# Performance work log

Measured on AMD Instinct MI355X. Metric: run time of the kernel, lower is better.

The kernel has to match this reference:

```python
import jax, jax.numpy as jnp
import numpy as np

T, B, H, W = 4, 8, 480, 640
N = 4_000_000


def setup_inputs() -> dict:
    key = jax.random.key(0)
    k1, k2, k3, k4 = jax.random.split(key, 4)
    # sorted batch ids (events grouped per sample)
    batch = jnp.sort(jax.random.randint(k1, (N,), 0, B)).astype(jnp.int32)
    # x,y normalized to [0,1]; t sorted globally => sorted within each batch
    xy = jax.random.uniform(k2, (N, 2), dtype=jnp.float32)
    t = jnp.sort(jax.random.uniform(k3, (N,), dtype=jnp.float32))
    pos = jnp.concatenate([xy, t[:, None]], axis=1)  # [N,3]
    feat = jax.random.normal(k4, (N, 1), dtype=jnp.float32)  # polarity = feat[:,0] > 0
    return {"pos": pos, "feat": feat, "batch": batch}


def _voxelize(pos, feat, batch):
    n = pos.shape[0]
    bids = jnp.arange(B, dtype=batch.dtype)
    left = jnp.searchsorted(batch, bids, side="left")
    right = jnporig = jnp.searchsorted(batch, bids, side="right")
    first = jnp.clip(left, 0, n - 1)
    last = jnp.clip(right - 1, 0, n - 1)

    t = pos[:, 2]
    cnt = right - left
    # torch: if t[-1] == t[0] (and >=2 events), bump last event's t by 1
    bump = ((cnt >= 2) & (t[last] == t[first])).astype(t.dtype)
    t = t.at[last].add(bump)

    t0b = t[first]                       # per-batch t[0]
    denom = t[last] - t0b                # per-batch t[-1]-t[0]
    denom = jnp.where(denom == 0, 1.0, denom)  # guard degenerate segments
    tn = (T - 1) * (t - t0b[batch]) / denom[batch]  # [N]

    xf = pos[:, 0] * (W - 1)
    yf = pos[:, 1] * (H - 1)
    x0 = xf.astype(jnp.int32)
    y0 = yf.astype(jnp.int32)
    t0 = tn.astype(jnp.int32)
    ch = jnp.where(feat[:, 0] > 0, 0, 1).astype(jnp.int32)  # pos->chan0, neg->chan1

    # 8 trilinear corners: offsets in {0,1}^3, shape [8,1] broadcast vs [N]
    offs = jnp.array([[dx, dy, dt] for dx in (0, 1) for dy in (0, 1) for dt in (0, 1)], dtype=jnp.int32)
    xl = x0[None, :] + offs[:, 0:1]  # [8,N]
    yl = y0[None, :] + offs[:, 1:2]
    tl = t0[None, :] + offs[:, 2:3]

    m = (xl >= 0) & (xl < W) & (yl >= 0) & (yl < H) & (tl >= 0) & (tl < T)
    w = (1 - jnp.abs(xl - xf[None, :])) * (1 - jnp.abs(yl - yf[None, :])) * (1 - jnp.abs(tl - tn[None, :]))

    bb = batch[None, :].astype(jnp.int32)
    idx = (((tl * B + bb) * 2 + ch[None, :]) * H + yl) * W + xl  # flat into [T,B,2,H,W]
    idx = jnp.where(m, idx, 0)
    w = jnp.where(m, w, 0.0)

    out = jnp.zeros(T * B * 2 * H * W, dtype=jnp.float32).at[idx.ravel()].add(w.ravel())
    return out.reshape(T, B, 2, H, W)


def reference(pos, feat, batch) -> jnp.ndarray:
    return _voxelize(pos, feat, batch)
```

## Files before the change

kernel.cpp:

```cpp
#include <hip/hip_runtime.h>

#define TT 4
#define BB 8
#define HH 480
#define WW 640
#define YSTR 4
#define NYB (HH/YSTR)
#define NBINS2 (BB*TT*NYB)
#define CAP2 1792
#define PPB2 2048
#define FTH 512
#define ITER (PPB2/FTH)
#define SBINS 1024
#define RROWS 4
#define NSTRIPE (HH/RROWS)
#define GTH 512
#define FXSCALE 524288.0f
#define FXINV (1.0f/524288.0f)

struct BatchParams { float t0b; float denom; int last; int bump; };

__global__ void setup_kernel(const float* __restrict__ pos, const int* __restrict__ batch,
                             int n, BatchParams* __restrict__ bp) {
    int b = threadIdx.x;
    if (b >= BB) return;
    int lo = 0, hi = n;
    while (lo < hi) { int mid = (lo + hi) >> 1; if (batch[mid] < b) lo = mid + 1; else hi = mid; }
    int left = lo;
    lo = left; hi = n;
    while (lo < hi) { int mid = (lo + hi) >> 1; if (batch[mid] <= b) lo = mid + 1; else hi = mid; }
    int right = lo;
    int first = min(max(left, 0), n - 1);
    int last  = min(max(right - 1, 0), n - 1);
    int cnt   = right - left;
    float tf = pos[(size_t)first * 3 + 2];
    float tl = pos[(size_t)last  * 3 + 2];
    int bump = (cnt >= 2 && tl == tf) ? 1 : 0;
    float d = (tl + (float)bump) - tf;
    if (d == 0.0f) d = 1.0f;
    bp[b].t0b = tf; bp[b].denom = d; bp[b].last = last; bp[b].bump = bump;
}

__device__ __forceinline__ int point_g(const BatchParams* sbp, const float* pos,
                                       const int* batch, int i, float* tn_out) {
    int b = batch[i];
    float t = pos[(size_t)i * 3 + 2];
    BatchParams p = sbp[b];
    if (p.bump && i == p.last) t += 1.0f;
    float tn = (float)(TT - 1) * (t - p.t0b) / p.denom;
    *tn_out = tn;
    return b * TT + (int)tn;
}

__global__ __launch_bounds__(FTH) void fill4_kernel(
        const float* __restrict__ pos, const float* __restrict__ feat,
        const int* __restrict__ batch, const BatchParams* __restrict__ bp,
        unsigned int* __restrict__ cursor, uint2* __restrict__ binidx, int n) {
    __shared__ uint2 stage[PPB2];
    __shared__ unsigned int addrbuf[PPB2];
    __shared__ unsigned int hist[SBINS];
    __shared__ int          dlt[SBINS];
    __shared__ unsigned int ps[FTH];
    __shared__ unsigned int totloc;
    __shared__ BatchParams sbp[BB];
    int tid = threadIdx.x;
    if (tid < BB) sbp[tid] = bp[tid];
    hist[tid] = 0; hist[tid + FTH] = 0;
    __syncthreads();

    int lo = blockIdx.x * PPB2;
    float tnd;
    int g_lo = point_g(sbp, pos, batch, lo, &tnd);
    int binbase_lo = g_lo * NYB;

    unsigned int rx[ITER], ry[ITER];
    int keyv[ITER];
    #pragma unroll
    for (int it = 0; it < ITER; ++it) {
        int i = lo + it * FTH + tid;
        keyv[it] = -1;
        if (i < n) {
            float tn;
            int g = point_g(sbp, pos, batch, i, &tn);
            float xf = pos[(size_t)i * 3 + 0] * (float)(WW - 1);
            float yf = pos[(size_t)i * 3 + 1] * (float)(HH - 1);
            int x0 = (int)xf, y0 = (int)yf, t0 = (int)tn;
            float fx = xf - (float)x0;
            float fy = yf - (float)y0;
            float ft = tn - (float)t0;
            unsigned int ch = (feat[i] > 0.0f) ? 0u : 1u;
            rx[it] = (unsigned int)x0 | (ch << 10) | ((unsigned int)y0 << 11)
                   | (((unsigned int)(fx * 4095.0f + 0.5f)) << 20);
            ry[it] = ((unsigned int)(fy * 65535.0f + 0.5f))
                   | (((unsigned int)(ft * 65535.0f + 0.5f)) << 16);
            keyv[it] = g * NYB + (y0 >> 2);
            int lb = keyv[it] - binbase_lo;
            if (lb < SBINS) atomicAdd(&hist[lb], 1u);
        }
    }
    __syncthreads();
    unsigned int c0 = hist[2 * tid], c1 = hist[2 * tid + 1];
    unsigned int sum = c0 + c1;
    ps[tid] = sum;
    __syncthreads();
    for (int off = 1; off < FTH; off <<= 1) {
        unsigned int v = (tid >= off) ? ps[tid - off] : 0u;
        __syncthreads();
        ps[tid] += v;
        __syncthreads();
    }
    unsigned int base = ps[tid] - sum;
    if (tid == FTH - 1) totloc = ps[FTH - 1];
    {
        unsigned int lp0 = base, lp1 = base + c0;
        int bin0 = binbase_lo + 2 * tid;
        unsigned int gb0 = 0, gb1 = 0;
        if (c0 && bin0     < NBINS2) gb0 = atomicAdd(&cursor[bin0],     c0);
        if (c1 && bin0 + 1 < NBINS2) gb1 = atomicAdd(&cursor[bin0 + 1], c1);
        dlt[2 * tid]     = (int)gb0 - (int)lp0;
        dlt[2 * tid + 1] = (int)gb1 - (int)lp1;
        hist[2 * tid] = lp0; hist[2 * tid + 1] = lp1;
    }
    __syncthreads();
    #pragma unroll
    for (int it = 0; it < ITER; ++it) {
        if (keyv[it] >= 0) {
            int lb = keyv[it] - binbase_lo;
            uint2 rec; rec.x = rx[it]; rec.y = ry[it];
            if (lb < SBINS) {
                unsigned int p = atomicAdd(&hist[lb], 1u);
                int off = dlt[lb] + (int)p;
                stage[p] = rec;
                addrbuf[p] = ((unsigned int)off < CAP2)
                           ? (unsigned int)keyv[it] * CAP2 + (unsigned int)off
                           : 0xFFFFFFFFu;
            } else {
                unsigned int slot = atomicAdd(&cursor[keyv[it]], 1u);
                if (slot < CAP2) binidx[(size_t)keyv[it] * CAP2 + slot] = rec;
            }
        }
    }
    __syncthreads();
    unsigned int tot = totloc;
    for (unsigned int k = tid; k < tot; k += FTH) {
        unsigned int a = addrbuf[k];
        if (a != 0xFFFFFFFFu) binidx[a] = stage[k];
    }
}

__device__ __forceinline__ void gather_own(unsigned long long* tile, uint2 rec, int q) {
    int x0 = (int)(rec.x & 1023u);
    int ch = (int)((rec.x >> 10) & 1u);
    int r_in = (int)((rec.x >> 11) & 3u);
    float fx = (float)((rec.x >> 20) & 4095u) * (1.0f / 4095.0f);
    float fy = (float)(rec.y & 65535u) * (1.0f / 65535.0f);
    float ft = (float)(rec.y >> 16) * (1.0f / 65535.0f);
    float wt = q ? (1.0f - ft) : ft;
    float w0 = wt * (1.0f - fy);
    unsigned long long* rowp = &tile[(ch * RROWS + r_in) * WW + x0];
    unsigned long long p0 =
          (unsigned long long)(unsigned int)fmaf(w0 * (1.0f - fx), FXSCALE, 0.5f)
        | ((unsigned long long)(unsigned int)fmaf(w0 * fx, FXSCALE, 0.5f) << 32);
    atomicAdd(rowp, p0);
    if (r_in < RROWS - 1) {
        float w1 = wt * fy;
        unsigned long long p1 =
              (unsigned long long)(unsigned int)fmaf(w1 * (1.0f - fx), FXSCALE, 0.5f)
            | ((unsigned long long)(unsigned int)fmaf(w1 * fx, FXSCALE, 0.5f) << 32);
        atomicAdd(rowp + WW, p1);
    }
}

__device__ __forceinline__ void gather_nb(unsigned long long* tile, uint2 rec, int q) {
    if (((rec.x >> 11) & 3u) != 3u) return;
    int x0 = (int)(rec.x & 1023u);
    int ch = (int)((rec.x >> 10) & 1u);
    float fx = (float)((rec.x >> 20) & 4095u) * (1.0f / 4095.0f);
    float fy = (float)(rec.y & 65535u) * (1.0f / 65535.0f);
    float ft = (float)(rec.y >> 16) * (1.0f / 65535.0f);
    float wt = q ? (1.0f - ft) : ft;
    float w1 = wt * fy;
    unsigned long long p1 =
          (unsigned long long)(unsigned int)fmaf(w1 * (1.0f - fx), FXSCALE, 0.5f)
        | ((unsigned long long)(unsigned int)fmaf(w1 * fx, FXSCALE, 0.5f) << 32);
    atomicAdd(&tile[(ch * RROWS + 0) * WW + x0], p1);
}

__global__ __launch_bounds__(GTH) void gather6_kernel(
        const unsigned int* __restrict__ cursor, const uint2* __restrict__ binidx,
        float* __restrict__ out) {
    __shared__ unsigned long long tile[2 * RROWS * WW];
    __shared__ unsigned int cnt[4];
    int bid = blockIdx.x;
    int s  = bid % NSTRIPE;
    int bt = bid / NSTRIPE;
    int tl = bt % TT;
    int b  = bt / TT;
    int r0 = s * RROWS;
    int tid = threadIdx.x;

    if (tid < 4) {
        int q  = tid & 1;
        int nb = tid >> 1;
        int t0r = tl - 1 + q;
        int sp  = s - nb;
        unsigned int c = 0;
        if (t0r >= 0 && sp >= 0)
            c = min(cursor[(b * TT + t0r) * NYB + sp], (unsigned int)CAP2);
        cnt[tid] = c;
    }
    for (int k = tid; k < 2 * RROWS * WW; k += GTH) tile[k] = 0ull;
    __syncthreads();

    #pragma unroll
    for (int q = 0; q < 2; ++q) {
        int t0r = tl - 1 + q;
        if (t0r < 0) continue;
        unsigned int base = (unsigned int)((b * TT + t0r) * NYB + s) * CAP2;
        unsigned int c = cnt[q];
        unsigned int m = tid;
        if (m < c) {
            uint2 rec = binidx[base + m];
            for (;;) {
                unsigned int m2 = m + GTH;
                bool has2 = m2 < c;
                uint2 rec2;
                if (has2) rec2 = binidx[base + m2];
                gather_own(tile, rec, q);
                if (!has2) break;
                rec = rec2; m = m2;
            }
        }
    }
    #pragma unroll
    for (int q = 0; q < 2; ++q) {
        int t0r = tl - 1 + q;
        if (t0r < 0 || s == 0) continue;
        unsigned int base = (unsigned int)((b * TT + t0r) * NYB + (s - 1)) * CAP2;
        unsigned int c = cnt[2 + q];
        unsigned int m = tid;
        if (m < c) {
            uint2 rec = binidx[base + m];
            for (;;) {
                unsigned int m2 = m + GTH;
                bool has2 = m2 < c;
                uint2 rec2;
                if (has2) rec2 = binidx[base + m2];
                gather_nb(tile, rec, q);
                if (!has2) break;
                rec = rec2; m = m2;
            }
        }
    }
    __syncthreads();
    const unsigned int* t32 = (const unsigned int*)tile;
    const int QUADS = 2 * RROWS * WW / 4;
    for (int qd = tid; qd < QUADS; qd += GTH) {
        int e = qd * 4;
        uint4 A = *(const uint4*)&t32[e * 2];
        uint4 B = *(const uint4*)&t32[e * 2 + 4];
        unsigned int cc = (e % WW == 0) ? 0u : t32[e * 2 - 1];
        float4 v;
        v.x = (float)(A.x + cc)  * FXINV;
        v.y = (float)(A.z + A.y) * FXINV;
        v.z = (float)(B.x + A.w) * FXINV;
        v.w = (float)(B.z + B.y) * FXINV;
        int ch  = e / (RROWS * WW);
        int rem = e % (RROWS * WW);
        int r   = rem / WW;
        int x   = rem % WW;
        *(float4*)&out[((((size_t)tl * BB + b) * 2 + ch) * HH + (r0 + r)) * WW + x] = v;
    }
}

__global__ void voxel_kernel(const float* __restrict__ pos, const float* __restrict__ feat,
                             const int* __restrict__ batch, const BatchParams* __restrict__ bp,
                             float* __restrict__ out, int n) {
    __shared__ BatchParams sbp[BB];
    if (threadIdx.x < BB) sbp[threadIdx.x] = bp[threadIdx.x];
    __syncthreads();
    int i = blockIdx.x * blockDim.x + threadIdx.x;
    if (i >= n) return;
    int b = batch[i];
    float x = pos[(size_t)i * 3 + 0];
    float y = pos[(size_t)i * 3 + 1];
    float t = pos[(size_t)i * 3 + 2];
    BatchParams p = sbp[b];
    if (p.bump && i == p.last) t += 1.0f;
    float tn = (float)(TT - 1) * (t - p.t0b) / p.denom;
    float xf = x * (float)(WW - 1);
    float yf = y * (float)(HH - 1);
    int x0 = (int)xf, y0 = (int)yf, t0 = (int)tn;
    float fx = xf - (float)x0, fy = yf - (float)y0, ft = tn - (float)t0;
    int ch = (feat[i] > 0.0f) ? 0 : 1;
    float wx[2] = {1.0f - fx, fx};
    float wy[2] = {1.0f - fy, fy};
    float wt[2] = {1.0f - ft, ft};
    #pragma unroll
    for (int dt = 0; dt < 2; ++dt) {
        int tlc = t0 + dt;
        if (tlc < 0 || tlc >= TT) continue;
        #pragma unroll
        for (int dy = 0; dy < 2; ++dy) {
            int yl = y0 + dy;
            if (yl < 0 || yl >= HH) continue;
            #pragma unroll
            for (int dx = 0; dx < 2; ++dx) {
                int xl = x0 + dx;
                if (xl < 0 || xl >= WW) continue;
                float w = wx[dx] * wy[dy] * wt[dt];
                size_t idx = ((((size_t)tlc * BB + b) * 2 + ch) * (size_t)HH + yl) * (size_t)WW + xl;
                atomicAdd(&out[idx], w);
            }
        }
    }
}

extern "C" void kernel_launch(void* const* d_in, const int* in_sizes, int n_in,
                              void* d_out, int out_size, void* d_ws, size_t ws_size,
                              hipStream_t stream) {
    const float* pos   = (const float*)d_in[0];
    const float* feat  = (const float*)d_in[1];
    const int*   batch = (const int*)d_in[2];
    float* out = (float*)d_out;
    int n = in_sizes[2];

    char* ws = (char*)d_ws;
    BatchParams* bp      = (BatchParams*)ws;
    unsigned int* cursor = (unsigned int*)(ws + 1024);
    uint2*        binidx = (uint2*)(ws + 65536);
    size_t need = 65536 + (size_t)NBINS2 * CAP2 * sizeof(uint2);

    if (ws_size >= need) {
        hipMemsetAsync(cursor, 0, NBINS2 * sizeof(unsigned int), stream);
        setup_kernel<<<1, 64, 0, stream>>>(pos, batch, n, bp);
        int nblocks = (n + PPB2 - 1) / PPB2;
        fill4_kernel<<<nblocks, FTH, 0, stream>>>(pos, feat, batch, bp, cursor, binidx, n);
        gather6_kernel<<<BB * TT * NSTRIPE, GTH, 0, stream>>>(cursor, binidx, out);
    } else {
        hipMemsetAsync(d_out, 0, (size_t)out_size * sizeof(float), stream);
        setup_kernel<<<1, 64, 0, stream>>>(pos, batch, n, bp);
        int blocks = (n + 255) / 256;
        voxel_kernel<<<blocks, 256, 0, stream>>>(pos, feat, batch, bp, out, n);
    }
}
```

Baseline: 92.50 us.

## Duplicate halo-row events into neighbor bins at fill time; single-pass gather

The fill kernel now writes a second, halo-flagged record for each event on the last row of its 4-row stripe into the next stripe's bin. The gather kernel then reads only its own bin instead of also scanning the whole previous stripe's bin just to pick out its bottom-row events. The block-wide prefix scan is also replaced by a wavefront shuffle scan plus per-wave totals. Bin capacity and staging buffers are enlarged and points per block reduced to make room for the extra records. The cost is more fill writes and larger workspace traffic in exchange for less redundant gather reading.

```diff
diff --git a/kernel.cpp b/kernel.cpp
--- a/kernel.cpp
+++ b/kernel.cpp
@@ -7,14 +7,16 @@
 #define YSTR 4
 #define NYB (HH/YSTR)
 #define NBINS2 (BB*TT*NYB)
-#define CAP2 1792
-#define PPB2 2048
+#define CAP2 2048
+#define PPB2 1536
 #define FTH 512
 #define ITER (PPB2/FTH)
 #define SBINS 1024
+#define STAGECAP 2112
 #define RROWS 4
 #define NSTRIPE (HH/RROWS)
 #define GTH 512
+#define SPILL 0x80000000u
 #define FXSCALE 524288.0f
 #define FXINV (1.0f/524288.0f)
 
@@ -52,20 +54,20 @@
     return b * TT + (int)tn;
 }
 
-__global__ __launch_bounds__(FTH) void fill4_kernel(
+__global__ __launch_bounds__(FTH) void fill5_kernel(
         const float* __restrict__ pos, const float* __restrict__ feat,
         const int* __restrict__ batch, const BatchParams* __restrict__ bp,
         unsigned int* __restrict__ cursor, uint2* __restrict__ binidx, int n) {
-    __shared__ uint2 stage[PPB2];
-    __shared__ unsigned int addrbuf[PPB2];
+    __shared__ uint2 stage[STAGECAP];
+    __shared__ unsigned int addrbuf[STAGECAP];
     __shared__ unsigned int hist[SBINS];
     __shared__ int          dlt[SBINS];
-    __shared__ unsigned int ps[FTH];
+    __shared__ unsigned int wavesum[8];
     __shared__ unsigned int totloc;
     __shared__ BatchParams sbp[BB];
     int tid = threadIdx.x;
     if (tid < BB) sbp[tid] = bp[tid];
-    hist[tid] = 0; hist[tid + FTH] = 0;
+    hist[2 * tid] = 0; hist[2 * tid + 1] = 0;
     __syncthreads();
 
     int lo = blockIdx.x * PPB2;
@@ -73,12 +75,12 @@
     int g_lo = point_g(sbp, pos, batch, lo, &tnd);
     int binbase_lo = g_lo * NYB;
 
-    unsigned int rx[ITER], ry[ITER];
-    int keyv[ITER];
+    unsigned int rx[ITER], ry[ITER], pm[ITER], ph[ITER];
+    int keyv[ITER], hkeyv[ITER];
     #pragma unroll
     for (int it = 0; it < ITER; ++it) {
         int i = lo + it * FTH + tid;
-        keyv[it] = -1;
+        keyv[it] = -1; hkeyv[it] = -1;
         if (i < n) {
             float tn;
             int g = point_g(sbp, pos, batch, i, &tn);
@@ -89,28 +91,40 @@
             float fy = yf - (float)y0;
             float ft = tn - (float)t0;
             unsigned int ch = (feat[i] > 0.0f) ? 0u : 1u;
-            rx[it] = (unsigned int)x0 | (ch << 10) | ((unsigned int)y0 << 11)
+            unsigned int rin = (unsigned int)(y0 & 3);
+            rx[it] = (unsigned int)x0 | (ch << 10) | (rin << 11)
                    | (((unsigned int)(fx * 4095.0f + 0.5f)) << 20);
             ry[it] = ((unsigned int)(fy * 65535.0f + 0.5f))
                    | (((unsigned int)(ft * 65535.0f + 0.5f)) << 16);
-            keyv[it] = g * NYB + (y0 >> 2);
-            int lb = keyv[it] - binbase_lo;
-            if (lb < SBINS) atomicAdd(&hist[lb], 1u);
+            int key = g * NYB + (y0 >> 2);
+            keyv[it] = key;
+            int lb = key - binbase_lo;
+            pm[it] = (lb < SBINS) ? atomicAdd(&hist[lb], 1u) : SPILL;
+            if (rin == 3u && (y0 >> 2) < NYB - 1) {
+                hkeyv[it] = key + 1;
+                int lbh = lb + 1;
+                ph[it] = (lbh < SBINS) ? atomicAdd(&hist[lbh], 1u) : SPILL;
+            }
         }
     }
     __syncthreads();
     unsigned int c0 = hist[2 * tid], c1 = hist[2 * tid + 1];
     unsigned int sum = c0 + c1;
-    ps[tid] = sum;
-    __syncthreads();
-    for (int off = 1; off < FTH; off <<= 1) {
-        unsigned int v = (tid >= off) ? ps[tid - off] : 0u;
-        __syncthreads();
-        ps[tid] += v;
-        __syncthreads();
-    }
-    unsigned int base = ps[tid] - sum;
-    if (tid == FTH - 1) totloc = ps[FTH - 1];
+    int lane = tid & 63, wid = tid >> 6;
+    unsigned int scan = sum;
+    #pragma unroll
+    for (int off = 1; off < 64; off <<= 1) {
+        unsigned int v = __shfl_up(scan, off, 64);
+        if (lane >= off) scan += v;
+    }
+    if (lane == 63) wavesum[wid] = scan;
+    __syncthreads();
+    unsigned int woff = 0;
+    #pragma unroll
+    for (int w = 0; w < 8; ++w) woff += (w < wid) ? wavesum[w] : 0u;
+    unsigned int incl = woff + scan;
+    unsigned int base = incl - sum;
+    if (tid == FTH - 1) totloc = incl;
     {
         unsigned int lp0 = base, lp1 = base + c0;
         int bin0 = binbase_lo + 2 * tid;
@@ -124,57 +138,43 @@
     __syncthreads();
     #pragma unroll
     for (int it = 0; it < ITER; ++it) {
-        if (keyv[it] >= 0) {
-            int lb = keyv[it] - binbase_lo;
-            uint2 rec; rec.x = rx[it]; rec.y = ry[it];
-            if (lb < SBINS) {
-                unsigned int p = atomicAdd(&hist[lb], 1u);
-                int off = dlt[lb] + (int)p;
-                stage[p] = rec;
-                addrbuf[p] = ((unsigned int)off < CAP2)
-                           ? (unsigned int)keyv[it] * CAP2 + (unsigned int)off
-                           : 0xFFFFFFFFu;
+        if (keyv[it] < 0) continue;
+        #pragma unroll
+        for (int h = 0; h < 2; ++h) {
+            int key = h ? hkeyv[it] : keyv[it];
+            if (key < 0) continue;
+            unsigned int p = h ? ph[it] : pm[it];
+            uint2 rec; rec.x = h ? (rx[it] | (1u << 13)) : rx[it]; rec.y = ry[it];
+            if (p & SPILL) {
+                unsigned int slot = atomicAdd(&cursor[key], 1u);
+                if (slot < CAP2) binidx[(size_t)key * CAP2 + slot] = rec;
             } else {
-                unsigned int slot = atomicAdd(&cursor[keyv[it]], 1u);
-                if (slot < CAP2) binidx[(size_t)keyv[it] * CAP2 + slot] = rec;
+                int lb = key - binbase_lo;
+                unsigned int sl = hist[lb] + p;
+                unsigned int off = (unsigned int)(dlt[lb] + (int)sl);
+                if (sl < STAGECAP) {
+                    stage[sl] = rec;
+                    addrbuf[sl] = (off < CAP2) ? (unsigned int)key * CAP2 + off
+                                               : 0xFFFFFFFFu;
+                } else if (off < CAP2) {
+                    binidx[(size_t)key * CAP2 + off] = rec;
+                }
             }
         }
     }
     __syncthreads();
-    unsigned int tot = totloc;
+    unsigned int tot = min(totloc, (unsigned int)STAGECAP);
     for (unsigned int k = tid; k < tot; k += FTH) {
         unsigned int a = addrbuf[k];
         if (a != 0xFFFFFFFFu) binidx[a] = stage[k];
     }
 }
 
-__device__ __forceinline__ void gather_own(unsigned long long* tile, uint2 rec, int q) {
-    int x0 = (int)(rec.x & 1023u);
-    int ch = (int)((rec.x >> 10) & 1u);
-    int r_in = (int)((rec.x >> 11) & 3u);
-    float fx = (float)((rec.x >> 20) & 4095u) * (1.0f / 4095.0f);
-    float fy = (float)(rec.y & 65535u) * (1.0f / 65535.0f);
-    float ft = (float)(rec.y >> 16) * (1.0f / 65535.0f);
-    float wt = q ? (1.0f - ft) : ft;
-    float w0 = wt * (1.0f - fy);
-    unsigned long long* rowp = &tile[(ch * RROWS + r_in) * WW + x0];
-    unsigned long long p0 =
-          (unsigned long long)(unsigned int)fmaf(w0 * (1.0f - fx), FXSCALE, 0.5f)
-        | ((unsigned long long)(unsigned int)fmaf(w0 * fx, FXSCALE, 0.5f) << 32);
-    atomicAdd(rowp, p0);
-    if (r_in < RROWS - 1) {
-        float w1 = wt * fy;
-        unsigned long long p1 =
-              (unsigned long long)(unsigned int)fmaf(w1 * (1.0f - fx), FXSCALE, 0.5f)
-            | ((unsigned long long)(unsigned int)fmaf(w1 * fx, FXSCALE, 0.5f) << 32);
-        atomicAdd(rowp + WW, p1);
-    }
-}
-
-__device__ __forceinline__ void gather_nb(unsigned long long* tile, uint2 rec, int q) {
-    if (((rec.x >> 11) & 3u) != 3u) return;
-    int x0 = (int)(rec.x & 1023u);
-    int ch = (int)((rec.x >> 10) & 1u);
+__device__ __forceinline__ void gather_rec(unsigned long long* tile, uint2 rec, int q) {
+    int x0   = (int)(rec.x & 1023u);
+    int ch   = (int)((rec.x >> 10) & 1u);
+    int rin  = (int)((rec.x >> 11) & 3u);
+    int halo = (int)((rec.x >> 13) & 1u);
     float fx = (float)((rec.x >> 20) & 4095u) * (1.0f / 4095.0f);
     float fy = (float)(rec.y & 65535u) * (1.0f / 65535.0f);
     float ft = (float)(rec.y >> 16) * (1.0f / 65535.0f);
@@ -183,14 +183,24 @@
     unsigned long long p1 =
           (unsigned long long)(unsigned int)fmaf(w1 * (1.0f - fx), FXSCALE, 0.5f)
         | ((unsigned long long)(unsigned int)fmaf(w1 * fx, FXSCALE, 0.5f) << 32);
-    atomicAdd(&tile[(ch * RROWS + 0) * WW + x0], p1);
-}
-
-__global__ __launch_bounds__(GTH) void gather6_kernel(
+    if (halo) {
+        atomicAdd(&tile[(ch * RROWS) * WW + x0], p1);
+    } else {
+        float w0 = wt * (1.0f - fy);
+        unsigned long long p0 =
+              (unsigned long long)(unsigned int)fmaf(w0 * (1.0f - fx), FXSCALE, 0.5f)
+            | ((unsigned long long)(unsigned int)fmaf(w0 * fx, FXSCALE, 0.5f) << 32);
+        unsigned long long* rowp = &tile[(ch * RROWS + rin) * WW + x0];
+        atomicAdd(rowp, p0);
+        if (rin < RROWS - 1) atomicAdd(rowp + WW, p1);
+    }
+}
+
+__global__ __launch_bounds__(GTH) void gather7_kernel(
         const unsigned int* __restrict__ cursor, const uint2* __restrict__ binidx,
         float* __restrict__ out) {
     __shared__ unsigned long long tile[2 * RROWS * WW];
-    __shared__ unsigned int cnt[4];
+    __shared__ unsigned int cnt[2];
     int bid = blockIdx.x;
     int s  = bid % NSTRIPE;
     int bt = bid / NSTRIPE;
@@ -199,14 +209,10 @@
     int r0 = s * RROWS;
     int tid = threadIdx.x;
 
-    if (tid < 4) {
-        int q  = tid & 1;
-        int nb = tid >> 1;
-        int t0r = tl - 1 + q;
-        int sp  = s - nb;
+    if (tid < 2) {
+        int t0r = tl - 1 + tid;
         unsigned int c = 0;
-        if (t0r >= 0 && sp >= 0)
-            c = min(cursor[(b * TT + t0r) * NYB + sp], (unsigned int)CAP2);
+        if (t0r >= 0) c = min(cursor[(b * TT + t0r) * NYB + s], (unsigned int)CAP2);
         cnt[tid] = c;
     }
     for (int k = tid; k < 2 * RROWS * WW; k += GTH) tile[k] = 0ull;
@@ -226,27 +232,7 @@
                 bool has2 = m2 < c;
                 uint2 rec2;
                 if (has2) rec2 = binidx[base + m2];
-                gather_own(tile, rec, q);
-                if (!has2) break;
-                rec = rec2; m = m2;
-            }
-        }
-    }
-    #pragma unroll
-    for (int q = 0; q < 2; ++q) {
-        int t0r = tl - 1 + q;
-        if (t0r < 0 || s == 0) continue;
-        unsigned int base = (unsigned int)((b * TT + t0r) * NYB + (s - 1)) * CAP2;
-        unsigned int c = cnt[2 + q];
-        unsigned int m = tid;
-        if (m < c) {
-            uint2 rec = binidx[base + m];
-            for (;;) {
-                unsigned int m2 = m + GTH;
-                bool has2 = m2 < c;
-                uint2 rec2;
-                if (has2) rec2 = binidx[base + m2];
-                gather_nb(tile, rec, q);
+                gather_rec(tile, rec, q);
                 if (!has2) break;
                 rec = rec2; m = m2;
             }
@@ -335,8 +321,8 @@
         hipMemsetAsync(cursor, 0, NBINS2 * sizeof(unsigned int), stream);
         setup_kernel<<<1, 64, 0, stream>>>(pos, batch, n, bp);
         int nblocks = (n + PPB2 - 1) / PPB2;
-        fill4_kernel<<<nblocks, FTH, 0, stream>>>(pos, feat, batch, bp, cursor, binidx, n);
-        gather6_kernel<<<BB * TT * NSTRIPE, GTH, 0, stream>>>(cursor, binidx, out);
+        fill5_kernel<<<nblocks, FTH, 0, stream>>>(pos, feat, batch, bp, cursor, binidx, n);
+        gather7_kernel<<<BB * TT * NSTRIPE, GTH, 0, stream>>>(cursor, binidx, out);
     } else {
         hipMemsetAsync(d_out, 0, (size_t)out_size * sizeof(float), stream);
         setup_kernel<<<1, 64, 0, stream>>>(pos, batch, n, bp);
```

New measurement: 92.04 us. About the same (-0.5%).
